# Performance work log

Hardware: AMD Instinct MI355X
Metric: run time of the kernel (lower is better)

Reference implementation:

```python
import jax, jax.numpy as jnp
import numpy as np

B, I, O, D = 8, 16, 16, 512
BASIS = 5

def setup_inputs() -> dict:
    key = jax.random.key(0)
    k1, k2, k3 = jax.random.split(key, 3)
    x = jax.random.normal(k1, (B, I, D), dtype=jnp.float32)
    fan_in = BASIS * I  # kaiming_uniform(a=sqrt(5)) on (O, 5I, 1, 1) -> bound = 1/sqrt(fan_in)
    bound = 1.0 / np.sqrt(fan_in)
    weight = jax.random.uniform(k2, (O, BASIS * I), dtype=jnp.float32, minval=-bound, maxval=bound)
    bias = jax.random.uniform(k3, (O,), dtype=jnp.float32, minval=-bound, maxval=bound)
    return {"x": x, "weight": weight, "bias": bias}

def reference(x, weight, bias):
    # x: (B, I, D); weight: (O, 5*I); bias: (O,)
    # Equivariant 1->2 basis ops (normalize=False), fused with the 1x1-conv channel
    # contraction instead of materializing the (B, 5I, D, D) concat:
    #   op1 = diag_embed(x); op2 = row-broadcast(x); op3 = col-broadcast(x);
    #   op4 = diag_embed(sum(x)); op5 = full-broadcast(sum(x))
    b_, i_, d_ = x.shape
    o_ = weight.shape[0]
    w = weight.reshape(o_, BASIS, i_)  # channel layout of the concat: [op1|op2|op3|op4|op5]
    s = x.sum(axis=-1)                                     # (B, I)
    y1 = jnp.einsum('oi,bid->bod', w[:, 0], x)             # diagonal term
    y2 = jnp.einsum('oi,bid->bod', w[:, 1], x)             # row broadcast term
    y3 = jnp.einsum('oi,bid->bod', w[:, 2], x)             # col broadcast term
    y4 = jnp.einsum('oi,bi->bo', w[:, 3], s)               # sum on diagonal
    y5 = jnp.einsum('oi,bi->bo', w[:, 4], s)               # sum everywhere
    out = y2[..., :, None] + y3[..., None, :] + y5[..., None, None]  # (B, O, D, D)
    diag = y1 + y4[..., None]                              # (B, O, D)
    out = out + jnp.eye(d_, dtype=x.dtype) * diag[..., :, None]
    return out + bias[None, :, None, None]
```

## Files before the change

kernel.cpp:

```cpp
#include <hip/hip_runtime.h>

#define NB 8
#define NI 16
#define NO 16
#define ND 512

__global__ __launch_bounds__(256) void leq_precompute(
    const float* __restrict__ x, const float* __restrict__ weight,
    const float* __restrict__ bias, float* __restrict__ rowv,
    float* __restrict__ colv, float* __restrict__ diagv)
{
    const int bo = blockIdx.x;
    const int b  = bo >> 4;
    const int o  = bo & 15;
    const int t  = threadIdx.x;

    const float* wbase = weight + o * (5 * NI);
    const float* xb    = x + b * (NI * ND);

    const int d0 = t, d1 = t + 256;
    float acc1a = 0.f, acc2a = 0.f, acc3a = 0.f;
    float acc1b = 0.f, acc2b = 0.f, acc3b = 0.f;
    float p4 = 0.f, p5 = 0.f;

    #pragma unroll
    for (int i = 0; i < NI; ++i) {
        const float w0 = wbase[0 * NI + i];
        const float w1 = wbase[1 * NI + i];
        const float w2 = wbase[2 * NI + i];
        const float w3 = wbase[3 * NI + i];
        const float w4 = wbase[4 * NI + i];
        const float xa = xb[i * ND + d0];
        const float xc = xb[i * ND + d1];
        acc1a += w0 * xa; acc2a += w1 * xa; acc3a += w2 * xa;
        acc1b += w0 * xc; acc2b += w1 * xc; acc3b += w2 * xc;
        const float xs = xa + xc;
        p4 += w3 * xs; p5 += w4 * xs;
    }

    #pragma unroll
    for (int off = 32; off > 0; off >>= 1) {
        p4 += __shfl_down(p4, off, 64);
        p5 += __shfl_down(p5, off, 64);
    }
    __shared__ float red4[4], red5[4];
    const int wave = t >> 6, lane = t & 63;
    if (lane == 0) { red4[wave] = p4; red5[wave] = p5; }
    __syncthreads();
    const float y4 = red4[0] + red4[1] + red4[2] + red4[3];
    const float y5 = red5[0] + red5[1] + red5[2] + red5[3];

    const float base = y5 + bias[o];
    float* rv = rowv  + bo * ND;
    float* cv = colv  + bo * ND;
    float* dv = diagv + bo * ND;
    rv[d0] = acc2a + base; rv[d1] = acc2b + base;
    cv[d0] = acc3a;        cv[d1] = acc3b;
    dv[d0] = acc1a + y4;   dv[d1] = acc1b + y4;
}

__global__ __launch_bounds__(256) void leq_write(
    const float* __restrict__ rowv, const float* __restrict__ colv,
    const float* __restrict__ diagv, float4* __restrict__ out)
{
    const int gid = blockIdx.x * 256 + threadIdx.x;
    const int c4 = gid & 127;
    const int r  = (gid >> 7) & 511;
    const int bo = gid >> 16;

    const float rvd = rowv[(bo << 9) + r];
    const float dvv = diagv[(bo << 9) + r];
    const float4 cv = reinterpret_cast<const float4*>(colv)[(bo << 7) + c4];

    const int dcol = r - (c4 << 2);
    float4 res;
    res.x = rvd + cv.x + ((dcol == 0) ? dvv : 0.0f);
    res.y = rvd + cv.y + ((dcol == 1) ? dvv : 0.0f);
    res.z = rvd + cv.z + ((dcol == 2) ? dvv : 0.0f);
    res.w = rvd + cv.w + ((dcol == 3) ? dvv : 0.0f);
    out[gid] = res;
}

extern "C" void kernel_launch(void* const* d_in, const int* in_sizes, int n_in,
                              void* d_out, int out_size, void* d_ws, size_t ws_size,
                              hipStream_t stream) {
    const float* x      = (const float*)d_in[0];
    const float* weight = (const float*)d_in[1];
    const float* bias   = (const float*)d_in[2];

    float* ws    = (float*)d_ws;
    float* rowv  = ws;
    float* colv  = ws + NB * NO * ND;
    float* diagv = ws + 2 * NB * NO * ND;

    leq_precompute<<<NB * NO, 256, 0, stream>>>(x, weight, bias, rowv, colv, diagv);

    const int total4 = NB * NO * ND * (ND / 4);
    leq_write<<<total4 / 256, 256, 0, stream>>>(rowv, colv, diagv, (float4*)d_out);
}
```

Before: 31.55 us.

## Fuse precompute and broadcast-write kernels into one with shared-memory staging

Merges the two kernels into one. Each block recomputes the row, column and diagonal vectors for its (b,o) pair in shared memory, then writes a 32-row tile of the output. This removes the second kernel launch and the workspace round-trip through global memory. The cost is that the 16-channel contraction over x is recomputed 16 times per (b,o), once per row tile.

```diff
diff --git a/kernel.cpp b/kernel.cpp
--- a/kernel.cpp
+++ b/kernel.cpp
@@ -4,23 +4,32 @@
 #define NI 16
 #define NO 16
 #define ND 512
+#define ROWS 32
+#define RT   (ND / ROWS)
 
-__global__ __launch_bounds__(256) void leq_precompute(
+__global__ __launch_bounds__(256) void leq_fused(
     const float* __restrict__ x, const float* __restrict__ weight,
-    const float* __restrict__ bias, float* __restrict__ rowv,
-    float* __restrict__ colv, float* __restrict__ diagv)
+    const float* __restrict__ bias, float4* __restrict__ out)
 {
-    const int bo = blockIdx.x;
-    const int b  = bo >> 4;
-    const int o  = bo & 15;
-    const int t  = threadIdx.x;
+    const int blk = blockIdx.x;
+    const int rt  = blk & (RT - 1);
+    const int bo  = blk >> 4;
+    const int b   = bo >> 4;
+    const int o   = bo & 15;
+    const int t   = threadIdx.x;
+
+    __shared__ __align__(16) float colvS[ND];
+    __shared__ float rowfS[ND];
+    __shared__ float diagfS[ND];
+    __shared__ float rwS[ROWS], dgS[ROWS];
+    __shared__ float red4[4], red5[4];
 
     const float* wbase = weight + o * (5 * NI);
     const float* xb    = x + b * (NI * ND);
 
     const int d0 = t, d1 = t + 256;
-    float acc1a = 0.f, acc2a = 0.f, acc3a = 0.f;
-    float acc1b = 0.f, acc2b = 0.f, acc3b = 0.f;
+    float a1a = 0.f, a2a = 0.f, a3a = 0.f;
+    float a1b = 0.f, a2b = 0.f, a3b = 0.f;
     float p4 = 0.f, p5 = 0.f;
 
     #pragma unroll
@@ -32,53 +41,56 @@
         const float w4 = wbase[4 * NI + i];
         const float xa = xb[i * ND + d0];
         const float xc = xb[i * ND + d1];
-        acc1a += w0 * xa; acc2a += w1 * xa; acc3a += w2 * xa;
-        acc1b += w0 * xc; acc2b += w1 * xc; acc3b += w2 * xc;
+        a1a += w0 * xa; a2a += w1 * xa; a3a += w2 * xa;
+        a1b += w0 * xc; a2b += w1 * xc; a3b += w2 * xc;
         const float xs = xa + xc;
         p4 += w3 * xs; p5 += w4 * xs;
     }
+    colvS[d0]  = a3a; colvS[d1]  = a3b;
+    rowfS[d0]  = a2a; rowfS[d1]  = a2b;
+    diagfS[d0] = a1a; diagfS[d1] = a1b;
 
     #pragma unroll
     for (int off = 32; off > 0; off >>= 1) {
         p4 += __shfl_down(p4, off, 64);
         p5 += __shfl_down(p5, off, 64);
     }
-    __shared__ float red4[4], red5[4];
     const int wave = t >> 6, lane = t & 63;
     if (lane == 0) { red4[wave] = p4; red5[wave] = p5; }
     __syncthreads();
+
     const float y4 = red4[0] + red4[1] + red4[2] + red4[3];
     const float y5 = red5[0] + red5[1] + red5[2] + red5[3];
+    const float base = y5 + bias[o];
+    if (t < ROWS) {
+        const int r = rt * ROWS + t;
+        rwS[t] = rowfS[r] + base;
+        dgS[t] = diagfS[r] + y4;
+    }
+    __syncthreads();
 
-    const float base = y5 + bias[o];
-    float* rv = rowv  + bo * ND;
-    float* cv = colv  + bo * ND;
-    float* dv = diagv + bo * ND;
-    rv[d0] = acc2a + base; rv[d1] = acc2b + base;
-    cv[d0] = acc3a;        cv[d1] = acc3b;
-    dv[d0] = acc1a + y4;   dv[d1] = acc1b + y4;
-}
+    const float4* colv4 = reinterpret_cast<const float4*>(colvS);
+    const int out_base = bo * (ND * (ND / 4)) + rt * ROWS * (ND / 4);
 
-__global__ __launch_bounds__(256) void leq_write(
-    const float* __restrict__ rowv, const float* __restrict__ colv,
-    const float* __restrict__ diagv, float4* __restrict__ out)
-{
-    const int gid = blockIdx.x * 256 + threadIdx.x;
-    const int c4 = gid & 127;
-    const int r  = (gid >> 7) & 511;
-    const int bo = gid >> 16;
+    #pragma unroll 4
+    for (int k = 0; k < ROWS * (ND / 4) / 256; ++k) {
+        const int idx = k * 256 + t;
+        const int c4  = idx & 127;
+        const int rl  = idx >> 7;
+        const int r   = rt * ROWS + rl;
 
-    const float rvd = rowv[(bo << 9) + r];
-    const float dvv = diagv[(bo << 9) + r];
-    const float4 cv = reinterpret_cast<const float4*>(colv)[(bo << 7) + c4];
+        const float  rv = rwS[rl];
+        const float  dv = dgS[rl];
+        const float4 cv = colv4[c4];
 
-    const int dcol = r - (c4 << 2);
-    float4 res;
-    res.x = rvd + cv.x + ((dcol == 0) ? dvv : 0.0f);
-    res.y = rvd + cv.y + ((dcol == 1) ? dvv : 0.0f);
-    res.z = rvd + cv.z + ((dcol == 2) ? dvv : 0.0f);
-    res.w = rvd + cv.w + ((dcol == 3) ? dvv : 0.0f);
-    out[gid] = res;
+        const int dcol = r - (c4 << 2);
+        float4 res;
+        res.x = rv + cv.x + ((dcol == 0) ? dv : 0.0f);
+        res.y = rv + cv.y + ((dcol == 1) ? dv : 0.0f);
+        res.z = rv + cv.z + ((dcol == 2) ? dv : 0.0f);
+        res.w = rv + cv.w + ((dcol == 3) ? dv : 0.0f);
+        out[out_base + idx] = res;
+    }
 }
 
 extern "C" void kernel_launch(void* const* d_in, const int* in_sizes, int n_in,
@@ -88,13 +100,5 @@
     const float* weight = (const float*)d_in[1];
     const float* bias   = (const float*)d_in[2];
 
-    float* ws    = (float*)d_ws;
-    float* rowv  = ws;
-    float* colv  = ws + NB * NO * ND;
-    float* diagv = ws + 2 * NB * NO * ND;
-
-    leq_precompute<<<NB * NO, 256, 0, stream>>>(x, weight, bias, rowv, colv, diagv);
-
-    const int total4 = NB * NO * ND * (ND / 4);
-    leq_write<<<total4 / 256, 256, 0, stream>>>(rowv, colv, diagv, (float4*)d_out);
+    leq_fused<<<NB * NO * RT, 256, 0, stream>>>(x, weight, bias, (float4*)d_out);
 }
```

Result: faster. 27.49 us (-12.9%).
